# Kernel tuning notes

Hardware: AMD Instinct MI355X
Metric: run time of the kernel (lower is better)

## Reference

```python
import jax, jax.numpy as jnp
import numpy as np

B, E, N, F = 8, 2048, 2048, 128

def setup_inputs() -> dict:
    key = jax.random.key(0)
    k1, k2, k3, k4 = jax.random.split(key, 4)
    node_embeddings = jax.random.normal(k1, (B, N, F), dtype=jnp.float32)
    adj = jax.random.randint(k2, (B, E, N), -1, 3).astype(jnp.float32)
    W = jax.random.normal(k3, (F, F), dtype=jnp.float32) * (1.0 / np.sqrt(F))
    b = jax.random.normal(k4, (F,), dtype=jnp.float32) * 0.01
    return {"node_embeddings": node_embeddings, "adj": adj, "W": W, "b": b}

def reference(node_embeddings, adj, W, b):
    # adj_target: 1 where adj == -1, else 0
    adj_target = (adj == -1).astype(node_embeddings.dtype)          # [B, E, N]
    norm = jnp.sum(adj_target, axis=-1, keepdims=True)               # [B, E, 1]
    norm = jnp.where(norm == 0, 1.0, norm)
    # masked-mean aggregation of neighbor vertices into hyperedges
    message_vertex = jnp.matmul(adj_target, node_embeddings) / norm  # [B, E, F]
    # linear (torch Linear: x @ W.T + b) + relu
    hyperedge_embeddings = jax.nn.relu(jnp.matmul(message_vertex, W.T) + b)
    return hyperedge_embeddings
```

## Files before the change

### kernel.cpp

```cpp
#include <hip/hip_runtime.h>
#include <hip/hip_bf16.h>

#define B_ 8
#define E_ 2048
#define N_ 2048
#define F_ 128

#define BM 32
#define BK 64
#define AP 72
#define BP 72
#define WP 136
#define MP 136

using bf16x8 = __bf16 __attribute__((ext_vector_type(8)));
using fx4    = float __attribute__((ext_vector_type(4)));

__global__ __launch_bounds__(256) void prep_node(const float* __restrict__ node,
                                                 __bf16* __restrict__ nodeT) {
    __shared__ __align__(16) __bf16 tile[F_][72];
    const int bid = blockIdx.x;
    const int b  = bid >> 5;
    const int n0 = (bid & 31) * 64;
    const int t  = threadIdx.x;

#pragma unroll
    for (int p = 0; p < 8; ++p) {
        int idx = t + 256 * p;
        int n   = idx >> 5;
        int f4  = (idx & 31) * 4;
        float4 v = *(const float4*)&node[((size_t)b * N_ + n0 + n) * F_ + f4];
        tile[f4 + 0][n] = (__bf16)v.x;
        tile[f4 + 1][n] = (__bf16)v.y;
        tile[f4 + 2][n] = (__bf16)v.z;
        tile[f4 + 3][n] = (__bf16)v.w;
    }
    __syncthreads();
#pragma unroll
    for (int p = 0; p < 4; ++p) {
        int idx = t + 256 * p;
        int f   = idx >> 3;
        int n8  = (idx & 7) * 8;
        uint4 v = *(const uint4*)&tile[f][n8];
        *(uint4*)&nodeT[((size_t)b * F_ + f) * N_ + n0 + n8] = v;
    }
}

__global__ __launch_bounds__(256) void prep_w(const float* __restrict__ W,
                                              __bf16* __restrict__ Wb) {
    int idx = blockIdx.x * 256 + threadIdx.x;
    float4 v = *(const float4*)&W[idx * 4];
    __bf16 o[4] = {(__bf16)v.x, (__bf16)v.y, (__bf16)v.z, (__bf16)v.w};
    *(uint2*)&Wb[idx * 4] = *(const uint2*)o;
}

__global__ __launch_bounds__(256) void v2h_main(const float* __restrict__ adj,
                                                const __bf16* __restrict__ nodeT,
                                                const __bf16* __restrict__ Wb,
                                                const float* __restrict__ bias,
                                                float* __restrict__ out) {
    __shared__ __align__(16) __bf16 smemAB[BM * AP + F_ * BP];
    __shared__ __align__(16) __bf16 Ws[F_ * WP];
    __shared__ float normS[BM];

    __bf16* As = smemAB;
    __bf16* Bs = smemAB + BM * AP;
    __bf16* Ms = smemAB;

    const int t    = threadIdx.x;
    const int bid  = blockIdx.x;
    const int b    = bid & 7;
    const int e0   = (bid >> 3) * BM;
    const int w    = t >> 6;
    const int lane = t & 63;
    const int wm   = w & 1;
    const int wf   = w >> 1;
    const int l15  = lane & 15;
    const int quad = lane >> 4;

#pragma unroll
    for (int p = 0; p < 8; ++p) {
        int idx = t + 256 * p;
        int g   = idx >> 4;
        int f8  = (idx & 15) * 8;
        *(uint4*)&Ws[g * WP + f8] = *(const uint4*)&Wb[g * F_ + f8];
    }

    fx4 acc[4] = {};
    float cnt0 = 0.f, cnt1 = 0.f;

    const int ar0 = t >> 4;
    const int ac  = (t & 15) * 4;
    const float*  adjR0 = adj + ((size_t)b * E_ + e0 + ar0) * N_;
    const float*  adjR1 = adjR0 + (size_t)16 * N_;
    const __bf16* nTB   = nodeT + (size_t)b * F_ * N_;

    for (int k0 = 0; k0 < N_; k0 += BK) {
        float4 a0 = *(const float4*)(adjR0 + k0 + ac);
        float4 a1 = *(const float4*)(adjR1 + k0 + ac);
        uint4 bv[4];
#pragma unroll
        for (int p = 0; p < 4; ++p) {
            int idx = t + 256 * p;
            int f   = idx >> 3;
            int k8  = (idx & 7) * 8;
            bv[p] = *(const uint4*)&nTB[(size_t)f * N_ + k0 + k8];
        }

        __syncthreads();

        {
            float m0 = (a0.x == -1.f) ? 1.f : 0.f;
            float m1 = (a0.y == -1.f) ? 1.f : 0.f;
            float m2 = (a0.z == -1.f) ? 1.f : 0.f;
            float m3 = (a0.w == -1.f) ? 1.f : 0.f;
            cnt0 += m0 + m1 + m2 + m3;
            __bf16 pk[4] = {(__bf16)m0, (__bf16)m1, (__bf16)m2, (__bf16)m3};
            *(uint2*)&As[ar0 * AP + ac] = *(const uint2*)pk;
        }
        {
            float m0 = (a1.x == -1.f) ? 1.f : 0.f;
            float m1 = (a1.y == -1.f) ? 1.f : 0.f;
            float m2 = (a1.z == -1.f) ? 1.f : 0.f;
            float m3 = (a1.w == -1.f) ? 1.f : 0.f;
            cnt1 += m0 + m1 + m2 + m3;
            __bf16 pk[4] = {(__bf16)m0, (__bf16)m1, (__bf16)m2, (__bf16)m3};
            *(uint2*)&As[(ar0 + 16) * AP + ac] = *(const uint2*)pk;
        }
#pragma unroll
        for (int p = 0; p < 4; ++p) {
            int idx = t + 256 * p;
            int f   = idx >> 3;
            int k8  = (idx & 7) * 8;
            *(uint4*)&Bs[f * BP + k8] = bv[p];
        }

        __syncthreads();

#pragma unroll
        for (int ks = 0; ks < 2; ++ks) {
            bf16x8 af = *(const bf16x8*)&As[(16 * wm + l15) * AP + ks * 32 + quad * 8];
#pragma unroll
            for (int ft = 0; ft < 4; ++ft) {
                bf16x8 bf = *(const bf16x8*)&Bs[(wf * 64 + ft * 16 + l15) * BP + ks * 32 + quad * 8];
                acc[ft] = __builtin_amdgcn_mfma_f32_16x16x32_bf16(af, bf, acc[ft], 0, 0, 0);
            }
        }
    }

#pragma unroll
    for (int m = 1; m < 16; m <<= 1) {
        cnt0 += __shfl_xor(cnt0, m, 16);
        cnt1 += __shfl_xor(cnt1, m, 16);
    }
    if ((t & 15) == 0) {
        normS[ar0]      = fmaxf(cnt0, 1.f);
        normS[ar0 + 16] = fmaxf(cnt1, 1.f);
    }
    __syncthreads();

    const int rbase = 16 * wm + quad * 4;
    float rn[4];
#pragma unroll
    for (int r = 0; r < 4; ++r) rn[r] = 1.f / normS[rbase + r];
#pragma unroll
    for (int ft = 0; ft < 4; ++ft) {
        int fcol = wf * 64 + ft * 16 + l15;
#pragma unroll
        for (int r = 0; r < 4; ++r)
            Ms[(rbase + r) * MP + fcol] = (__bf16)(acc[ft][r] * rn[r]);
    }
    __syncthreads();

    fx4 acc2[4] = {};
#pragma unroll
    for (int ks = 0; ks < 4; ++ks) {
        bf16x8 af = *(const bf16x8*)&Ms[(16 * wm + l15) * MP + ks * 32 + quad * 8];
#pragma unroll
        for (int gt = 0; gt < 4; ++gt) {
            bf16x8 wfr = *(const bf16x8*)&Ws[(wf * 64 + gt * 16 + l15) * WP + ks * 32 + quad * 8];
            acc2[gt] = __builtin_amdgcn_mfma_f32_16x16x32_bf16(af, wfr, acc2[gt], 0, 0, 0);
        }
    }

#pragma unroll
    for (int gt = 0; gt < 4; ++gt) {
        int g = wf * 64 + gt * 16 + l15;
        float bb = bias[g];
#pragma unroll
        for (int r = 0; r < 4; ++r) {
            int e = e0 + rbase + r;
            float v = acc2[gt][r] + bb;
            out[((size_t)b * E_ + e) * F_ + g] = fmaxf(v, 0.f);
        }
    }
}

extern "C" void kernel_launch(void* const* d_in, const int* in_sizes, int n_in,
                              void* d_out, int out_size, void* d_ws, size_t ws_size,
                              hipStream_t stream) {
    const float* node = (const float*)d_in[0];
    const float* adj  = (const float*)d_in[1];
    const float* W    = (const float*)d_in[2];
    const float* bias = (const float*)d_in[3];
    float* out = (float*)d_out;

    __bf16* nodeT = (__bf16*)d_ws;
    __bf16* Wb    = (__bf16*)((char*)d_ws + (size_t)B_ * F_ * N_ * 2);

    prep_node<<<256, 256, 0, stream>>>(node, nodeT);
    prep_w<<<16, 256, 0, stream>>>(W, Wb);
    v2h_main<<<512, 256, 0, stream>>>(adj, nodeT, Wb, bias, out);
}
```

Measured before the change: 242.7 us.

## Halve row tile, prefetch next K tile in registers, drop W smem staging

The main kernel's row tile shrinks from 32 to 16 hyperedges per block, doubling the grid to 1024 blocks, and a launch-bounds occupancy hint is added. The adjacency and node tiles for the next K step are now loaded into registers while the current step computes. W is read directly from global memory instead of being staged in shared memory, which cuts LDS use. prep_node is rewritten to use a direct strided transpose without shared memory. The aim is more parallelism and better latency hiding on an adjacency-bandwidth-bound kernel, at the cost of reloading each node tile twice as often across blocks.

Result: slower. 613.9 us (+152.9%).

```diff
diff --git a/kernel.cpp b/kernel.cpp
--- a/kernel.cpp
+++ b/kernel.cpp
@@ -6,11 +6,10 @@
 #define N_ 2048
 #define F_ 128
 
-#define BM 32
+#define BM 16
 #define BK 64
 #define AP 72
 #define BP 72
-#define WP 136
 #define MP 136
 
 using bf16x8 = __bf16 __attribute__((ext_vector_type(8)));
@@ -18,32 +17,22 @@
 
 __global__ __launch_bounds__(256) void prep_node(const float* __restrict__ node,
                                                  __bf16* __restrict__ nodeT) {
-    __shared__ __align__(16) __bf16 tile[F_][72];
     const int bid = blockIdx.x;
-    const int b  = bid >> 5;
-    const int n0 = (bid & 31) * 64;
-    const int t  = threadIdx.x;
+    const int b   = bid & 7;
+    const int n0  = (bid >> 3) * 32;
+    const int t   = threadIdx.x;
+    const int f   = t & 127;
+    const int nb  = n0 + (t >> 7) * 16;
 
+    const float* src = node + ((size_t)b * N_ + nb) * F_ + f;
+    __bf16 h[16];
 #pragma unroll
-    for (int p = 0; p < 8; ++p) {
-        int idx = t + 256 * p;
-        int n   = idx >> 5;
-        int f4  = (idx & 31) * 4;
-        float4 v = *(const float4*)&node[((size_t)b * N_ + n0 + n) * F_ + f4];
-        tile[f4 + 0][n] = (__bf16)v.x;
-        tile[f4 + 1][n] = (__bf16)v.y;
-        tile[f4 + 2][n] = (__bf16)v.z;
-        tile[f4 + 3][n] = (__bf16)v.w;
-    }
-    __syncthreads();
-#pragma unroll
-    for (int p = 0; p < 4; ++p) {
-        int idx = t + 256 * p;
-        int f   = idx >> 3;
-        int n8  = (idx & 7) * 8;
-        uint4 v = *(const uint4*)&tile[f][n8];
-        *(uint4*)&nodeT[((size_t)b * F_ + f) * N_ + n0 + n8] = v;
-    }
+    for (int i = 0; i < 16; ++i)
+        h[i] = (__bf16)src[(size_t)i * F_];
+
+    __bf16* dst = nodeT + ((size_t)b * F_ + f) * N_ + nb;
+    *(uint4*)&dst[0] = *(const uint4*)&h[0];
+    *(uint4*)&dst[8] = *(const uint4*)&h[8];
 }
 
 __global__ __launch_bounds__(256) void prep_w(const float* __restrict__ W,
@@ -54,13 +43,12 @@
     *(uint2*)&Wb[idx * 4] = *(const uint2*)o;
 }
 
-__global__ __launch_bounds__(256) void v2h_main(const float* __restrict__ adj,
-                                                const __bf16* __restrict__ nodeT,
-                                                const __bf16* __restrict__ Wb,
-                                                const float* __restrict__ bias,
-                                                float* __restrict__ out) {
+__global__ __launch_bounds__(256, 4) void v2h_main(const float* __restrict__ adj,
+                                                   const __bf16* __restrict__ nodeT,
+                                                   const __bf16* __restrict__ Wb,
+                                                   const float* __restrict__ bias,
+                                                   float* __restrict__ out) {
     __shared__ __align__(16) __bf16 smemAB[BM * AP + F_ * BP];
-    __shared__ __align__(16) __bf16 Ws[F_ * WP];
     __shared__ float normS[BM];
 
     __bf16* As = smemAB;
@@ -71,121 +59,112 @@
     const int bid  = blockIdx.x;
     const int b    = bid & 7;
     const int e0   = (bid >> 3) * BM;
-    const int w    = t >> 6;
+    const int wf   = t >> 6;
     const int lane = t & 63;
-    const int wm   = w & 1;
-    const int wf   = w >> 1;
     const int l15  = lane & 15;
     const int quad = lane >> 4;
 
-#pragma unroll
-    for (int p = 0; p < 8; ++p) {
-        int idx = t + 256 * p;
-        int g   = idx >> 4;
-        int f8  = (idx & 15) * 8;
-        *(uint4*)&Ws[g * WP + f8] = *(const uint4*)&Wb[g * F_ + f8];
-    }
-
-    fx4 acc[4] = {};
-    float cnt0 = 0.f, cnt1 = 0.f;
+    fx4 acc[2] = {};
+    float cnt = 0.f;
 
     const int ar0 = t >> 4;
     const int ac  = (t & 15) * 4;
-    const float*  adjR0 = adj + ((size_t)b * E_ + e0 + ar0) * N_;
-    const float*  adjR1 = adjR0 + (size_t)16 * N_;
-    const __bf16* nTB   = nodeT + (size_t)b * F_ * N_;
+    const float*  adjR = adj + ((size_t)b * E_ + e0 + ar0) * N_;
+    const __bf16* nTB  = nodeT + (size_t)b * F_ * N_;
+
+    float4 aR = *(const float4*)(adjR + ac);
+    uint4 bR[4];
+#pragma unroll
+    for (int p = 0; p < 4; ++p) {
+        int idx = t + 256 * p;
+        int f   = idx >> 3;
+        int k8  = (idx & 7) * 8;
+        bR[p] = *(const uint4*)&nTB[(size_t)f * N_ + k8];
+    }
 
     for (int k0 = 0; k0 < N_; k0 += BK) {
-        float4 a0 = *(const float4*)(adjR0 + k0 + ac);
-        float4 a1 = *(const float4*)(adjR1 + k0 + ac);
-        uint4 bv[4];
+        const int kn = (k0 + BK) & (N_ - 1);
+        float4 aN = *(const float4*)(adjR + kn + ac);
+        uint4 bN[4];
 #pragma unroll
         for (int p = 0; p < 4; ++p) {
             int idx = t + 256 * p;
             int f   = idx >> 3;
             int k8  = (idx & 7) * 8;
-            bv[p] = *(const uint4*)&nTB[(size_t)f * N_ + k0 + k8];
+            bN[p] = *(const uint4*)&nTB[(size_t)f * N_ + kn + k8];
         }
 
         __syncthreads();
 
         {
-            float m0 = (a0.x == -1.f) ? 1.f : 0.f;
-            float m1 = (a0.y == -1.f) ? 1.f : 0.f;
-            float m2 = (a0.z == -1.f) ? 1.f : 0.f;
-            float m3 = (a0.w == -1.f) ? 1.f : 0.f;
-            cnt0 += m0 + m1 + m2 + m3;
+            float m0 = (aR.x == -1.f) ? 1.f : 0.f;
+            float m1 = (aR.y == -1.f) ? 1.f : 0.f;
+            float m2 = (aR.z == -1.f) ? 1.f : 0.f;
+            float m3 = (aR.w == -1.f) ? 1.f : 0.f;
+            cnt += m0 + m1 + m2 + m3;
             __bf16 pk[4] = {(__bf16)m0, (__bf16)m1, (__bf16)m2, (__bf16)m3};
             *(uint2*)&As[ar0 * AP + ac] = *(const uint2*)pk;
-        }
-        {
-            float m0 = (a1.x == -1.f) ? 1.f : 0.f;
-            float m1 = (a1.y == -1.f) ? 1.f : 0.f;
-            float m2 = (a1.z == -1.f) ? 1.f : 0.f;
-            float m3 = (a1.w == -1.f) ? 1.f : 0.f;
-            cnt1 += m0 + m1 + m2 + m3;
-            __bf16 pk[4] = {(__bf16)m0, (__bf16)m1, (__bf16)m2, (__bf16)m3};
-            *(uint2*)&As[(ar0 + 16) * AP + ac] = *(const uint2*)pk;
         }
 #pragma unroll
         for (int p = 0; p < 4; ++p) {
             int idx = t + 256 * p;
             int f   = idx >> 3;
             int k8  = (idx & 7) * 8;
-            *(uint4*)&Bs[f * BP + k8] = bv[p];
+            *(uint4*)&Bs[f * BP + k8] = bR[p];
         }
 
         __syncthreads();
 
 #pragma unroll
         for (int ks = 0; ks < 2; ++ks) {
-            bf16x8 af = *(const bf16x8*)&As[(16 * wm + l15) * AP + ks * 32 + quad * 8];
+            bf16x8 af = *(const bf16x8*)&As[l15 * AP + ks * 32 + quad * 8];
 #pragma unroll
-            for (int ft = 0; ft < 4; ++ft) {
-                bf16x8 bf = *(const bf16x8*)&Bs[(wf * 64 + ft * 16 + l15) * BP + ks * 32 + quad * 8];
+            for (int ft = 0; ft < 2; ++ft) {
+                bf16x8 bf = *(const bf16x8*)&Bs[(wf * 32 + ft * 16 + l15) * BP + ks * 32 + quad * 8];
                 acc[ft] = __builtin_amdgcn_mfma_f32_16x16x32_bf16(af, bf, acc[ft], 0, 0, 0);
             }
         }
+
+        aR = aN;
+#pragma unroll
+        for (int p = 0; p < 4; ++p) bR[p] = bN[p];
     }
 
 #pragma unroll
-    for (int m = 1; m < 16; m <<= 1) {
-        cnt0 += __shfl_xor(cnt0, m, 16);
-        cnt1 += __shfl_xor(cnt1, m, 16);
-    }
-    if ((t & 15) == 0) {
-        normS[ar0]      = fmaxf(cnt0, 1.f);
-        normS[ar0 + 16] = fmaxf(cnt1, 1.f);
-    }
+    for (int m = 1; m < 16; m <<= 1)
+        cnt += __shfl_xor(cnt, m);
+    if ((t & 15) == 0)
+        normS[ar0] = fmaxf(cnt, 1.f);
     __syncthreads();
 
-    const int rbase = 16 * wm + quad * 4;
+    const int rbase = quad * 4;
     float rn[4];
 #pragma unroll
     for (int r = 0; r < 4; ++r) rn[r] = 1.f / normS[rbase + r];
 #pragma unroll
-    for (int ft = 0; ft < 4; ++ft) {
-        int fcol = wf * 64 + ft * 16 + l15;
+    for (int ft = 0; ft < 2; ++ft) {
+        int fcol = wf * 32 + ft * 16 + l15;
 #pragma unroll
         for (int r = 0; r < 4; ++r)
             Ms[(rbase + r) * MP + fcol] = (__bf16)(acc[ft][r] * rn[r]);
     }
     __syncthreads();
 
-    fx4 acc2[4] = {};
+    fx4 acc2[2] = {};
 #pragma unroll
     for (int ks = 0; ks < 4; ++ks) {
-        bf16x8 af = *(const bf16x8*)&Ms[(16 * wm + l15) * MP + ks * 32 + quad * 8];
+        bf16x8 af = *(const bf16x8*)&Ms[l15 * MP + ks * 32 + quad * 8];
 #pragma unroll
-        for (int gt = 0; gt < 4; ++gt) {
-            bf16x8 wfr = *(const bf16x8*)&Ws[(wf * 64 + gt * 16 + l15) * WP + ks * 32 + quad * 8];
+        for (int gt = 0; gt < 2; ++gt) {
+            int g = wf * 32 + gt * 16 + l15;
+            bf16x8 wfr = *(const bf16x8*)&Wb[(size_t)g * F_ + ks * 32 + quad * 8];
             acc2[gt] = __builtin_amdgcn_mfma_f32_16x16x32_bf16(af, wfr, acc2[gt], 0, 0, 0);
         }
     }
 
 #pragma unroll
-    for (int gt = 0; gt < 4; ++gt) {
-        int g = wf * 64 + gt * 16 + l15;
+    for (int gt = 0; gt < 2; ++gt) {
+        int g = wf * 32 + gt * 16 + l15;
         float bb = bias[g];
 #pragma unroll
         for (int r = 0; r < 4; ++r) {
@@ -208,7 +187,7 @@
     __bf16* nodeT = (__bf16*)d_ws;
     __bf16* Wb    = (__bf16*)((char*)d_ws + (size_t)B_ * F_ * N_ * 2);
 
-    prep_node<<<256, 256, 0, stream>>>(node, nodeT);
+    prep_node<<<512, 256, 0, stream>>>(node, nodeT);
     prep_w<<<16, 256, 0, stream>>>(W, Wb);
-    v2h_main<<<512, 256, 0, stream>>>(adj, nodeT, Wb, bias, out);
+    v2h_main<<<1024, 256, 0, stream>>>(adj, nodeT, Wb, bias, out);
 }
```
